# Kernel optimization log

Hardware: AMD Instinct MI355X
Metric: run time of the kernel (lower is better)

The kernel has to match this reference:

```python
import jax, jax.numpy as jnp
import numpy as np

EMB = 1024
HEADS = 16
HEAD_DIM = EMB // HEADS


def setup_inputs() -> dict:
    key = jax.random.key(0)
    ks = jax.random.split(key, 9)
    s = 1.0 / np.sqrt(EMB)  # torch Linear default init scale (uniform), use normal*s for simplicity of magnitude
    x = jax.random.normal(ks[0], (2, 2048, EMB), dtype=jnp.float32)
    wQ = jax.random.uniform(ks[1], (EMB, EMB), jnp.float32, -s, s)
    bQ = jax.random.uniform(ks[2], (EMB,), jnp.float32, -s, s)
    wK = jax.random.uniform(ks[3], (EMB, EMB), jnp.float32, -s, s)
    bK = jax.random.uniform(ks[4], (EMB,), jnp.float32, -s, s)
    wV = jax.random.uniform(ks[5], (EMB, EMB), jnp.float32, -s, s)
    bV = jax.random.uniform(ks[6], (EMB,), jnp.float32, -s, s)
    wO = jax.random.uniform(ks[7], (EMB, EMB), jnp.float32, -s, s)
    bO = jax.random.uniform(ks[8], (EMB,), jnp.float32, -s, s)
    return {"x": x, "wQ": wQ, "bQ": bQ, "wK": wK, "bK": bK, "wV": wV, "bV": bV, "wO": wO, "bO": bO}


def reference(x, wQ, bQ, wK, bK, wV, bV, wO, bO):
    B, S, E = x.shape
    H, Dh = HEADS, HEAD_DIM
    # manual LayerNorm-like scaling; torch.std uses unbiased (ddof=1)
    mu = jnp.mean(x, axis=-1, keepdims=True)
    sd = jnp.std(x, axis=-1, keepdims=True, ddof=1)
    xn = (x - mu) / (sd + 1e-6)
    # torch Linear: y = x @ W.T + b
    q = (xn @ wQ.T + bQ).reshape(B, S, H, Dh).transpose(0, 2, 1, 3)  # [B,H,S,Dh]
    k = (xn @ wK.T + bK).reshape(B, S, H, Dh).transpose(0, 2, 1, 3)
    v = (xn @ wV.T + bV).reshape(B, S, H, Dh).transpose(0, 2, 1, 3)
    scores = jnp.einsum('bhsd,bhtd->bhst', q, k) / np.sqrt(Dh).astype(np.float32)
    A = jax.nn.softmax(scores, axis=-1)
    Hout = jnp.einsum('bhst,bhtd->bhsd', A, v)  # [B,H,S,Dh]
    Hout = Hout.transpose(0, 2, 1, 3).reshape(B, S, E)
    return Hout @ wO.T + bO
```

## Files before the change

kernel.cpp:

```cpp
#include <hip/hip_runtime.h>
#include <cstdint>
#include <cstddef>

typedef __bf16 bf16x8 __attribute__((ext_vector_type(8)));
typedef float f32x4 __attribute__((ext_vector_type(4)));
typedef unsigned short us4 __attribute__((ext_vector_type(4)));
typedef unsigned short us8 __attribute__((ext_vector_type(8)));
typedef unsigned int ui4 __attribute__((ext_vector_type(4)));
typedef unsigned short u16;

#define QSCALE 0.18033688011112042f

#define MFMA16(a, b, c) __builtin_amdgcn_mfma_f32_16x16x32_bf16((a), (b), (c), 0, 0, 0)
#define GLOAD16(g, l)                                                        \
  __builtin_amdgcn_global_load_lds(                                          \
      (const __attribute__((address_space(1))) void*)(g),                    \
      (__attribute__((address_space(3))) void*)(l), 16, 0, 0)

__device__ __forceinline__ u16 f2bf(float x) {
  unsigned int u = __float_as_uint(x);
  unsigned int r = u + 0x7fffu + ((u >> 16) & 1u);
  return (u16)(r >> 16);
}

__global__ __launch_bounds__(256) void prep_kernel(
    const float* __restrict__ x, const float* __restrict__ wq,
    const float* __restrict__ wk, const float* __restrict__ wv,
    const float* __restrict__ wo, u16* __restrict__ xn,
    u16* __restrict__ wdst) {
  const int bid = blockIdx.x;
  const int t = threadIdx.x;
  if (bid < 4096) {
    const int row = bid;
    const float* xr = x + (size_t)row * 1024;
    float4 v = *(const float4*)(xr + t * 4);
    float s = v.x + v.y + v.z + v.w;
    float s2 = v.x * v.x + v.y * v.y + v.z * v.z + v.w * v.w;
#pragma unroll
    for (int o = 32; o >= 1; o >>= 1) {
      s += __shfl_xor(s, o);
      s2 += __shfl_xor(s2, o);
    }
    __shared__ float red[8];
    const int wv_ = t >> 6, ln = t & 63;
    if (ln == 0) {
      red[wv_] = s;
      red[4 + wv_] = s2;
    }
    __syncthreads();
    s = red[0] + red[1] + red[2] + red[3];
    s2 = red[4] + red[5] + red[6] + red[7];
    const float mu = s * (1.0f / 1024.0f);
    float var = (s2 - 1024.0f * mu * mu) * (1.0f / 1023.0f);
    var = fmaxf(var, 0.0f);
    const float inv = 1.0f / (sqrtf(var) + 1e-6f);
    us4 o;
    o.x = f2bf((v.x - mu) * inv);
    o.y = f2bf((v.y - mu) * inv);
    o.z = f2bf((v.z - mu) * inv);
    o.w = f2bf((v.w - mu) * inv);
    *(us4*)(xn + (size_t)row * 1024 + t * 4) = o;
  } else {
    const int wid = bid - 4096;
    const int mat = wid >> 9, xi = wid & 511;
    const float* src = (mat == 0) ? wq : (mat == 1) ? wk : (mat == 2) ? wv : wo;
    const float sc = (mat == 0) ? QSCALE : 1.0f;
    u16* d = wdst + ((size_t)mat << 20);
    const size_t i = ((size_t)xi * 256 + t) * 8;
    float4 a = *(const float4*)(src + i);
    float4 b = *(const float4*)(src + i + 4);
    us8 o;
    o[0] = f2bf(a.x * sc);
    o[1] = f2bf(a.y * sc);
    o[2] = f2bf(a.z * sc);
    o[3] = f2bf(a.w * sc);
    o[4] = f2bf(b.x * sc);
    o[5] = f2bf(b.y * sc);
    o[6] = f2bf(b.z * sc);
    o[7] = f2bf(b.w * sc);
    *(us8*)(d + i) = o;
  }
}

__device__ __forceinline__ void gemm64_core(const u16* __restrict__ A,
                                            const u16* __restrict__ W,
                                            int m0, int n0,
                                            u16 (*As)[64 * 32],
                                            u16 (*Bs)[128 * 32],
                                            f32x4 acc[2][4]) {
  const int tid = threadIdx.x;
  const int lane = tid & 63, wave = tid >> 6;
  const int wm = wave >> 1, wn = wave & 1;
  const int lr = lane & 15, lg = lane >> 4;

  auto stage = [&](int buf, int kt) {
    {
      const int row = tid >> 2, ch = tid & 3;
      const int sc = ch ^ ((row >> 1) & 3);
      GLOAD16(A + (size_t)(m0 + row) * 1024 + kt * 32 + sc * 8,
              &As[buf][tid * 8]);
    }
#pragma unroll
    for (int i = 0; i < 2; i++) {
      const int idx = i * 256 + tid;
      const int row = idx >> 2, ch = idx & 3;
      const int sc = ch ^ ((row >> 1) & 3);
      GLOAD16(W + (size_t)(n0 + row) * 1024 + kt * 32 + sc * 8,
              &Bs[buf][idx * 8]);
    }
  };

  stage(0, 0);
  const int cs = (lg ^ ((lr >> 1) & 3)) * 8;
  int cur = 0;
  for (int kt = 0; kt < 32; ++kt) {
    __syncthreads();
    if (kt + 1 < 32) stage(cur ^ 1, kt + 1);
    bf16x8 af[2], bfr[4];
#pragma unroll
    for (int m = 0; m < 2; m++)
      af[m] = *(const bf16x8*)&As[cur][(wm * 32 + m * 16 + lr) * 32 + cs];
#pragma unroll
    for (int n = 0; n < 4; n++)
      bfr[n] = *(const bf16x8*)&Bs[cur][(wn * 64 + n * 16 + lr) * 32 + cs];
#pragma unroll
    for (int m = 0; m < 2; m++)
#pragma unroll
      for (int n = 0; n < 4; n++)
        acc[m][n] = MFMA16(af[m], bfr[n], acc[m][n]);
    cur ^= 1;
  }
}

__global__ __launch_bounds__(256, 5) void qkv_gemm(
    const u16* __restrict__ xn, const u16* __restrict__ Wall,
    const float* __restrict__ bQ, const float* __restrict__ bK,
    const float* __restrict__ bV, u16* __restrict__ Qb, u16* __restrict__ Kb,
    u16* __restrict__ VTb) {
  __shared__ u16 As[2][64 * 32];
  __shared__ u16 Bs[2][128 * 32];
  const int z = blockIdx.z;
  const u16* W = Wall + ((size_t)z << 20);
  const float* bias = (z == 0) ? bQ : (z == 1) ? bK : bV;
  const float bscale = (z == 0) ? QSCALE : 1.0f;
  const int m0 = blockIdx.x * 64, n0 = blockIdx.y * 128;
  f32x4 acc[2][4] = {};
  gemm64_core(xn, W, m0, n0, As, Bs, acc);

  const int lane = threadIdx.x & 63, wave = threadIdx.x >> 6;
  const int wm = wave >> 1, wn = wave & 1, lr = lane & 15, lg = lane >> 4;
  if (z == 2) {
#pragma unroll
    for (int n = 0; n < 4; n++) {
      const int col = n0 + wn * 64 + n * 16 + lr;
      const float bv = bias[col];
      const int hh = col >> 6, d = col & 63;
#pragma unroll
      for (int m = 0; m < 2; m++) {
        const int rb = m0 + wm * 32 + m * 16 + lg * 4;
#pragma unroll
        for (int j = 0; j < 4; j++) {
          const int row = rb + j;
          const int bb = row >> 11, s = row & 2047;
          VTb[(((size_t)(bb * 16 + hh) * 64 + d) << 11) + s] =
              f2bf(acc[m][n][j] + bv);
        }
      }
    }
  } else {
    u16* o = (z == 0) ? Qb : Kb;
#pragma unroll
    for (int n = 0; n < 4; n++) {
      const int col = n0 + wn * 64 + n * 16 + lr;
      const float bv = bias[col] * bscale;
#pragma unroll
      for (int m = 0; m < 2; m++) {
        const int rb = m0 + wm * 32 + m * 16 + lg * 4;
#pragma unroll
        for (int j = 0; j < 4; j++)
          o[(size_t)(rb + j) * 1024 + col] = f2bf(acc[m][n][j] + bv);
      }
    }
  }
}

__global__ __launch_bounds__(256, 5) void o_gemm(const u16* __restrict__ A,
                                                 const u16* __restrict__ W,
                                                 const float* __restrict__ bias,
                                                 float* __restrict__ out) {
  __shared__ u16 As[2][64 * 32];
  __shared__ u16 Bs[2][128 * 32];
  const int m0 = blockIdx.x * 64, n0 = blockIdx.y * 128;
  f32x4 acc[2][4] = {};
  gemm64_core(A, W, m0, n0, As, Bs, acc);
  const int lane = threadIdx.x & 63, wave = threadIdx.x >> 6;
  const int wm = wave >> 1, wn = wave & 1, lr = lane & 15, lg = lane >> 4;
#pragma unroll
  for (int n = 0; n < 4; n++) {
    const int col = n0 + wn * 64 + n * 16 + lr;
    const float bv = bias[col];
#pragma unroll
    for (int m = 0; m < 2; m++) {
      const int rb = m0 + wm * 32 + m * 16 + lg * 4;
#pragma unroll
      for (int j = 0; j < 4; j++)
        out[(size_t)(rb + j) * 1024 + col] = acc[m][n][j] + bv;
    }
  }
}

__global__ __launch_bounds__(256, 2) void attn_kernel(
    const u16* __restrict__ Qb, const u16* __restrict__ Kb,
    const u16* __restrict__ VTb, u16* __restrict__ Hb) {
  __shared__ u16 Ks[2][128 * 64];
  __shared__ u16 Vs[2][64 * 128];
  const int tid = threadIdx.x;
  const int wave = tid >> 6, lane = tid & 63;
  const int lr = lane & 15, lg = lane >> 4;
  const int qb = blockIdx.x, bh = blockIdx.y;
  const int b = bh >> 4, h = bh & 15;

  bf16x8 aq[2][2];
#pragma unroll
  for (int qg = 0; qg < 2; qg++) {
    const int qrow = b * 2048 + qb * 128 + wave * 32 + qg * 16 + lr;
    const u16* qsrc = Qb + (size_t)qrow * 1024 + h * 64 + lg * 8;
    aq[qg][0] = *(const bf16x8*)qsrc;
    aq[qg][1] = *(const bf16x8*)(qsrc + 32);
  }

  f32x4 oacc[2][4] = {};
  f32x4 lacc[2] = {};
  const ui4 ones_u = {0x3f803f80u, 0x3f803f80u, 0x3f803f80u, 0x3f803f80u};
  const bf16x8 ones = __builtin_bit_cast(bf16x8, ones_u);

  auto stage = [&](int buf, int kt) {
#pragma unroll
    for (int i = 0; i < 4; i++) {
      const int idx = i * 256 + tid;
      const int r = idx >> 3, c = idx & 7;
      GLOAD16(Kb + (size_t)(b * 2048 + kt * 128 + r) * 1024 + h * 64 +
                  (c ^ (r & 7)) * 8,
              &Ks[buf][idx * 8]);
    }
#pragma unroll
    for (int i = 0; i < 4; i++) {
      const int idx = i * 256 + tid;
      const int r = idx >> 4, c = idx & 15;
      GLOAD16(VTb + (size_t)(bh * 64 + r) * 2048 + kt * 128 +
                  (c ^ (r & 7)) * 8,
              &Vs[buf][idx * 8]);
    }
  };

  auto softpack = [&](f32x4 (&s)[8], ui4 (&pf)[4]) {
#pragma unroll
    for (int n = 0; n < 8; n++)
#pragma unroll
      for (int j = 0; j < 4; j++)
        s[n][j] = __builtin_amdgcn_exp2f(s[n][j]);
    unsigned int w[8][2];
#pragma unroll
    for (int n = 0; n < 8; n++) {
      asm("v_cvt_pk_bf16_f32 %0, %1, %2"
          : "=v"(w[n][0])
          : "v"(s[n][0]), "v"(s[n][1]));
      asm("v_cvt_pk_bf16_f32 %0, %1, %2"
          : "=v"(w[n][1])
          : "v"(s[n][2]), "v"(s[n][3]));
    }
#pragma unroll
    for (int ks = 0; ks < 4; ks++) {
      unsigned int pw[4];
#pragma unroll
      for (int rp = 0; rp < 2; rp++) {
        unsigned int a = w[2 * ks][rp], bb = w[2 * ks + 1][rp];
        asm("v_permlane32_swap_b32 %0, %1" : "+v"(a), "+v"(bb));
        asm("v_permlane16_swap_b32 %0, %1" : "+v"(a), "+v"(bb));
        pw[rp] = a;
        pw[2 + rp] = bb;
      }
      pf[ks] = (ui4){pw[0], pw[1], pw[2], pw[3]};
    }
  };

  stage(0, 0);
  int cur = 0;
  for (int kt = 0; kt < 16; ++kt) {
    __syncthreads();
    if (kt + 1 < 16) stage(cur ^ 1, kt + 1);

    f32x4 s0[8], s1[8];
#pragma unroll
    for (int n = 0; n < 8; n++) {
      s0[n] = (f32x4){0.f, 0.f, 0.f, 0.f};
      s1[n] = (f32x4){0.f, 0.f, 0.f, 0.f};
    }
    __builtin_amdgcn_s_setprio(1);
#pragma unroll
    for (int n = 0; n < 8; n++) {
      const int row = n * 16 + lr;
#pragma unroll
      for (int ks = 0; ks < 2; ks++) {
        const int byo = (ks * 64 + lg * 16) ^ ((row & 7) << 4);
        const bf16x8 kfr = *(const bf16x8*)&Ks[cur][row * 64 + (byo >> 1)];
        s0[n] = MFMA16(kfr, aq[0][ks], s0[n]);
        s1[n] = MFMA16(kfr, aq[1][ks], s1[n]);
      }
    }
    __builtin_amdgcn_s_setprio(0);

    ui4 pf0[4], pf1[4];
    softpack(s0, pf0);
    softpack(s1, pf1);

    __builtin_amdgcn_s_setprio(1);
#pragma unroll
    for (int ks = 0; ks < 4; ks++) {
      const bf16x8 p0 = __builtin_bit_cast(bf16x8, pf0[ks]);
      const bf16x8 p1 = __builtin_bit_cast(bf16x8, pf1[ks]);
#pragma unroll
      for (int n = 0; n < 4; n++) {
        const int row = n * 16 + lr;
        const int byo = (ks * 64 + lg * 16) ^ ((row & 7) << 4);
        const bf16x8 vb = *(const bf16x8*)&Vs[cur][row * 128 + (byo >> 1)];
        oacc[0][n] = MFMA16(p0, vb, oacc[0][n]);
        oacc[1][n] = MFMA16(p1, vb, oacc[1][n]);
      }
      lacc[0] = MFMA16(p0, ones, lacc[0]);
      lacc[1] = MFMA16(p1, ones, lacc[1]);
    }
    __builtin_amdgcn_s_setprio(0);
    cur ^= 1;
  }

#pragma unroll
  for (int qg = 0; qg < 2; qg++) {
    float rl[4];
#pragma unroll
    for (int j = 0; j < 4; j++) rl[j] = 1.0f / lacc[qg][j];
    const int hrow_base = b * 2048 + qb * 128 + wave * 32 + qg * 16 + lg * 4;
#pragma unroll
    for (int n = 0; n < 4; n++) {
      const int col = h * 64 + n * 16 + lr;
#pragma unroll
      for (int j = 0; j < 4; j++) {
        const float val = oacc[qg][n][j] * rl[j];
        Hb[(size_t)(hrow_base + j) * 1024 + col] = f2bf(val);
      }
    }
  }
}

extern "C" void kernel_launch(void* const* d_in, const int* in_sizes, int n_in,
                              void* d_out, int out_size, void* d_ws,
                              size_t ws_size, hipStream_t stream) {
  const float* x = (const float*)d_in[0];
  const float* wQ = (const float*)d_in[1];
  const float* bQ = (const float*)d_in[2];
  const float* wK = (const float*)d_in[3];
  const float* bK = (const float*)d_in[4];
  const float* wV = (const float*)d_in[5];
  const float* bV = (const float*)d_in[6];
  const float* wO = (const float*)d_in[7];
  const float* bO = (const float*)d_in[8];
  float* out = (float*)d_out;

  char* ws = (char*)d_ws;
  u16* xn = (u16*)(ws);
  u16* Wall = (u16*)(ws + ((size_t)8 << 20));
  u16* Qb = (u16*)(ws + ((size_t)16 << 20));
  u16* Kb = (u16*)(ws + ((size_t)24 << 20));
  u16* VTb = (u16*)(ws + ((size_t)32 << 20));
  u16* Hb = (u16*)(ws + ((size_t)40 << 20));

  prep_kernel<<<6144, 256, 0, stream>>>(x, wQ, wK, wV, wO, xn, Wall);
  qkv_gemm<<<dim3(64, 8, 3), 256, 0, stream>>>(xn, Wall, bQ, bK, bV, Qb, Kb,
                                               VTb);
  attn_kernel<<<dim3(16, 32), 256, 0, stream>>>(Qb, Kb, VTb, Hb);
  o_gemm<<<dim3(64, 8), 256, 0, stream>>>(Hb, Wall + ((size_t)3 << 20), bO,
                                          out);
}
```

Baseline: 119.7 us.

## Use single-buffered BK=64 k-loop for QKV projection GEMM

Replaces the double-buffered 32-wide k-step GEMM core in the QKV projection with a single-buffered core that stages 64-wide k tiles, using an XOR swizzle over 8 chunks. This halves the number of k iterations and barriers per tile and raises the occupancy hint from 5 to 6 blocks. In exchange, global loads no longer overlap with MFMA compute within a block, so latency hiding depends on other resident blocks. The O projection keeps the old double-buffered core.

```diff
diff --git a/kernel.cpp b/kernel.cpp
--- a/kernel.cpp
+++ b/kernel.cpp
@@ -82,6 +82,105 @@
   }
 }
 
+__device__ __forceinline__ void gemm_sbuf_core(const u16* __restrict__ A,
+                                               const u16* __restrict__ W,
+                                               int m0, int n0,
+                                               u16* __restrict__ As,
+                                               u16* __restrict__ Bs,
+                                               f32x4 acc[2][4]) {
+  const int tid = threadIdx.x;
+  const int lane = tid & 63, wave = tid >> 6;
+  const int wm = wave >> 1, wn = wave & 1;
+  const int lr = lane & 15, lg = lane >> 4;
+
+  for (int kt = 0; kt < 16; ++kt) {
+#pragma unroll
+    for (int i = 0; i < 2; i++) {
+      const int idx = i * 256 + tid;
+      const int r = idx >> 3, c = idx & 7;
+      GLOAD16(A + (size_t)(m0 + r) * 1024 + kt * 64 + (c ^ (r & 7)) * 8,
+              &As[idx * 8]);
+    }
+#pragma unroll
+    for (int i = 0; i < 4; i++) {
+      const int idx = i * 256 + tid;
+      const int r = idx >> 3, c = idx & 7;
+      GLOAD16(W + (size_t)(n0 + r) * 1024 + kt * 64 + (c ^ (r & 7)) * 8,
+              &Bs[idx * 8]);
+    }
+    __syncthreads();
+#pragma unroll
+    for (int ks = 0; ks < 2; ks++) {
+      const int co = ((ks * 4 + lg) ^ (lr & 7)) * 8;
+      bf16x8 af[2], bfr[4];
+#pragma unroll
+      for (int m = 0; m < 2; m++)
+        af[m] = *(const bf16x8*)&As[(wm * 32 + m * 16 + lr) * 64 + co];
+#pragma unroll
+      for (int n = 0; n < 4; n++)
+        bfr[n] = *(const bf16x8*)&Bs[(wn * 64 + n * 16 + lr) * 64 + co];
+#pragma unroll
+      for (int m = 0; m < 2; m++)
+#pragma unroll
+        for (int n = 0; n < 4; n++)
+          acc[m][n] = MFMA16(af[m], bfr[n], acc[m][n]);
+    }
+    __syncthreads();
+  }
+}
+
+__global__ __launch_bounds__(256, 6) void qkv_gemm(
+    const u16* __restrict__ xn, const u16* __restrict__ Wall,
+    const float* __restrict__ bQ, const float* __restrict__ bK,
+    const float* __restrict__ bV, u16* __restrict__ Qb, u16* __restrict__ Kb,
+    u16* __restrict__ VTb) {
+  __shared__ u16 As[64 * 64];
+  __shared__ u16 Bs[128 * 64];
+  const int z = blockIdx.z;
+  const u16* W = Wall + ((size_t)z << 20);
+  const float* bias = (z == 0) ? bQ : (z == 1) ? bK : bV;
+  const float bscale = (z == 0) ? QSCALE : 1.0f;
+  const int m0 = blockIdx.x * 64, n0 = blockIdx.y * 128;
+  f32x4 acc[2][4] = {};
+  gemm_sbuf_core(xn, W, m0, n0, As, Bs, acc);
+
+  const int lane = threadIdx.x & 63, wave = threadIdx.x >> 6;
+  const int wm = wave >> 1, wn = wave & 1, lr = lane & 15, lg = lane >> 4;
+  if (z == 2) {
+#pragma unroll
+    for (int n = 0; n < 4; n++) {
+      const int col = n0 + wn * 64 + n * 16 + lr;
+      const float bv = bias[col];
+      const int hh = col >> 6, d = col & 63;
+#pragma unroll
+      for (int m = 0; m < 2; m++) {
+        const int rb = m0 + wm * 32 + m * 16 + lg * 4;
+#pragma unroll
+        for (int j = 0; j < 4; j++) {
+          const int row = rb + j;
+          const int bb = row >> 11, s = row & 2047;
+          VTb[(((size_t)(bb * 16 + hh) * 64 + d) << 11) + s] =
+              f2bf(acc[m][n][j] + bv);
+        }
+      }
+    }
+  } else {
+    u16* o = (z == 0) ? Qb : Kb;
+#pragma unroll
+    for (int n = 0; n < 4; n++) {
+      const int col = n0 + wn * 64 + n * 16 + lr;
+      const float bv = bias[col] * bscale;
+#pragma unroll
+      for (int m = 0; m < 2; m++) {
+        const int rb = m0 + wm * 32 + m * 16 + lg * 4;
+#pragma unroll
+        for (int j = 0; j < 4; j++)
+          o[(size_t)(rb + j) * 1024 + col] = f2bf(acc[m][n][j] + bv);
+      }
+    }
+  }
+}
+
 __device__ __forceinline__ void gemm64_core(const u16* __restrict__ A,
                                             const u16* __restrict__ W,
                                             int m0, int n0,
@@ -129,58 +228,6 @@
       for (int n = 0; n < 4; n++)
         acc[m][n] = MFMA16(af[m], bfr[n], acc[m][n]);
     cur ^= 1;
-  }
-}
-
-__global__ __launch_bounds__(256, 5) void qkv_gemm(
-    const u16* __restrict__ xn, const u16* __restrict__ Wall,
-    const float* __restrict__ bQ, const float* __restrict__ bK,
-    const float* __restrict__ bV, u16* __restrict__ Qb, u16* __restrict__ Kb,
-    u16* __restrict__ VTb) {
-  __shared__ u16 As[2][64 * 32];
-  __shared__ u16 Bs[2][128 * 32];
-  const int z = blockIdx.z;
-  const u16* W = Wall + ((size_t)z << 20);
-  const float* bias = (z == 0) ? bQ : (z == 1) ? bK : bV;
-  const float bscale = (z == 0) ? QSCALE : 1.0f;
-  const int m0 = blockIdx.x * 64, n0 = blockIdx.y * 128;
-  f32x4 acc[2][4] = {};
-  gemm64_core(xn, W, m0, n0, As, Bs, acc);
-
-  const int lane = threadIdx.x & 63, wave = threadIdx.x >> 6;
-  const int wm = wave >> 1, wn = wave & 1, lr = lane & 15, lg = lane >> 4;
-  if (z == 2) {
-#pragma unroll
-    for (int n = 0; n < 4; n++) {
-      const int col = n0 + wn * 64 + n * 16 + lr;
-      const float bv = bias[col];
-      const int hh = col >> 6, d = col & 63;
-#pragma unroll
-      for (int m = 0; m < 2; m++) {
-        const int rb = m0 + wm * 32 + m * 16 + lg * 4;
-#pragma unroll
-        for (int j = 0; j < 4; j++) {
-          const int row = rb + j;
-          const int bb = row >> 11, s = row & 2047;
-          VTb[(((size_t)(bb * 16 + hh) * 64 + d) << 11) + s] =
-              f2bf(acc[m][n][j] + bv);
-        }
-      }
-    }
-  } else {
-    u16* o = (z == 0) ? Qb : Kb;
-#pragma unroll
-    for (int n = 0; n < 4; n++) {
-      const int col = n0 + wn * 64 + n * 16 + lr;
-      const float bv = bias[col] * bscale;
-#pragma unroll
-      for (int m = 0; m < 2; m++) {
-        const int rb = m0 + wm * 32 + m * 16 + lg * 4;
-#pragma unroll
-        for (int j = 0; j < 4; j++)
-          o[(size_t)(rb + j) * 1024 + col] = f2bf(acc[m][n][j] + bv);
-      }
-    }
   }
 }
 
```

Measured after the change: 128.8 us. 7.6% more time.
